# Performance work log

Measured on AMD Instinct MI355X. Metric: run time of the kernel, lower is better.

Reference implementation:

```python
import jax, jax.numpy as jnp
import numpy as np
import math

EMB = 1024
H = 8          # num_heads
HD = EMB // H // 2  # head_dim = 64
LAMBDA_INIT = 0.8
B, N = 2, 2048


def setup_inputs() -> dict:
    key = jax.random.key(0)
    ks = jax.random.split(key, 16)
    s = 1.0 / math.sqrt(EMB)
    d = {
        'q': jax.random.normal(ks[0], (B, N, EMB), jnp.float32),
        'k': jax.random.normal(ks[1], (B, N, EMB), jnp.float32),
        'v': jax.random.normal(ks[2], (B, N, EMB), jnp.float32),
        'Wq': jax.random.uniform(ks[3], (EMB, EMB), jnp.float32, -s, s),
        'bq': jax.random.uniform(ks[4], (EMB,), jnp.float32, -s, s),
        'Wk': jax.random.uniform(ks[5], (EMB, EMB), jnp.float32, -s, s),
        'bk': jax.random.uniform(ks[6], (EMB,), jnp.float32, -s, s),
        'Wv': jax.random.uniform(ks[7], (EMB, EMB), jnp.float32, -s, s),
        'bv': jax.random.uniform(ks[8], (EMB,), jnp.float32, -s, s),
        'Wo': jax.random.uniform(ks[9], (EMB, EMB), jnp.float32, -s, s),
        'bo': jax.random.uniform(ks[10], (EMB,), jnp.float32, -s, s),
        'lambda_q1': 0.1 * jax.random.normal(ks[11], (HD,), jnp.float32),
        'lambda_k1': 0.1 * jax.random.normal(ks[12], (HD,), jnp.float32),
        'lambda_q2': 0.1 * jax.random.normal(ks[13], (HD,), jnp.float32),
        'lambda_k2': 0.1 * jax.random.normal(ks[14], (HD,), jnp.float32),
    }
    return d


def reference(q, k, v, Wq, bq, Wk, bk, Wv, bv, Wo, bo,
              lambda_q1, lambda_k1, lambda_q2, lambda_k2):
    b, n, _ = q.shape
    # projections (torch Linear: x @ W.T + b)
    qp = q @ Wq.T + bq            # [b, n, EMB]
    kp = k @ Wk.T + bk
    vp = v @ Wv.T + bv
    # split into 2*H sub-heads of width HD for q/k; H heads of width 2*HD for v
    qh = qp.reshape(b, n, 2 * H, HD).transpose(0, 2, 1, 3)   # [b, 2H, n, HD]
    kh = kp.reshape(b, n, 2 * H, HD).transpose(0, 2, 1, 3)   # [b, 2H, n, HD]
    vh = vp.reshape(b, n, H, 2 * HD).transpose(0, 2, 1, 3)   # [b, H, n, 2HD]
    scale = 1.0 / math.sqrt(HD)
    attn = jnp.einsum('bhqd,bhkd->bhqk', qh, kh) * scale      # [b, 2H, n, n]
    attn = jax.nn.softmax(attn, axis=-1)
    lam1 = jnp.exp(jnp.sum(lambda_q1 * lambda_k1))
    lam2 = jnp.exp(jnp.sum(lambda_q2 * lambda_k2))
    lam = lam1 - lam2 + LAMBDA_INIT
    attn = attn.reshape(b, H, 2, n, n)
    diff = attn[:, :, 0] - lam * attn[:, :, 1]                # [b, H, n, n]
    out = jnp.einsum('bhqk,bhkd->bhqd', diff, vh)             # [b, H, n, 2HD]
    out = out.transpose(0, 2, 1, 3).reshape(b, n, H * 2 * HD)
    return out @ Wo.T + bo
```

## Files before the change

### kernel.cpp

```cpp
#include <hip/hip_runtime.h>
#include <stdint.h>


typedef __attribute__((ext_vector_type(8))) __bf16 bf16x8;
typedef __attribute__((ext_vector_type(4))) __bf16 bf16x4;
typedef __attribute__((ext_vector_type(4))) float f32x4;
typedef __attribute__((ext_vector_type(16))) float f32x16;
typedef __attribute__((ext_vector_type(8))) unsigned short u16x8;
typedef __attribute__((ext_vector_type(4))) unsigned short u16x4;
typedef __attribute__((ext_vector_type(4))) unsigned int u32x4;
typedef unsigned short u16;
typedef unsigned int u32;

#define EMB 1024
#define NSEQ 2048
#define NBATCH 2
#define NHEAD 8
#define MROWS (NBATCH*NSEQ)
#define QSCALE 0.18033688011112042f

__device__ __forceinline__ u16x4 pk4(float a, float b, float c, float d){
  bf16x4 h; h[0]=(__bf16)a; h[1]=(__bf16)b; h[2]=(__bf16)c; h[3]=(__bf16)d;
  return __builtin_bit_cast(u16x4, h);
}
__device__ __forceinline__ u16 bf1(float f){
  __bf16 h = (__bf16)f; return __builtin_bit_cast(unsigned short, h);
}
__device__ __forceinline__ u32 cvtpk(float lo, float hi){
  u32 r; asm("v_cvt_pk_bf16_f32 %0, %1, %2" : "=v"(r) : "v"(lo), "v"(hi)); return r;
}

__device__ __forceinline__ bf16x8 ld8(const u16* p){
  return __builtin_bit_cast(bf16x8, *(const u16x8*)p);
}

__device__ __forceinline__ void glds16(const u16* g, u16* l){
  __builtin_amdgcn_global_load_lds(
      (const __attribute__((address_space(1))) u32*)g,
      (__attribute__((address_space(3))) u32*)l, 16, 0, 0);
}

__global__ void cvt_k(const float* __restrict__ q, const float* __restrict__ k,
                      const float* __restrict__ v, const float* __restrict__ Wq,
                      const float* __restrict__ Wk, const float* __restrict__ Wv,
                      const float* __restrict__ Wo,
                      u16* qb, u16* kb, u16* vb, u16* Wqb, u16* Wkb, u16* Wvb, u16* Wob)
{
  const int NQ4 = (NBATCH*NSEQ*EMB)/4;
  const int NW4 = (EMB*EMB)/4;
  const int total = 3*NQ4 + 4*NW4;
  for (int i = blockIdx.x*blockDim.x + threadIdx.x; i < total; i += gridDim.x*blockDim.x){
    const float* src; u16* dst; int off;
    if (i < 3*NQ4){
      int t = i / NQ4; off = i - t*NQ4;
      src = t==0 ? q : (t==1 ? k : v);
      dst = t==0 ? qb : (t==1 ? kb : vb);
    } else {
      int j = i - 3*NQ4;
      int t = j / NW4; off = j - t*NW4;
      src = t==0 ? Wq : (t==1 ? Wk : (t==2 ? Wv : Wo));
      dst = t==0 ? Wqb : (t==1 ? Wkb : (t==2 ? Wvb : Wob));
    }
    f32x4 f = *((const f32x4*)src + off);
    *((u16x4*)dst + off) = pk4(f[0], f[1], f[2], f[3]);
  }
}

__global__ void lambda_k(const float* __restrict__ lq1, const float* __restrict__ lk1,
                         const float* __restrict__ lq2, const float* __restrict__ lk2,
                         float* lam)
{
  int l = threadIdx.x;
  float p1 = lq1[l]*lk1[l];
  float p2 = lq2[l]*lk2[l];
  #pragma unroll
  for (int m=1; m<64; m<<=1){ p1 += __shfl_xor(p1, m, 64); p2 += __shfl_xor(p2, m, 64); }
  if (l==0) lam[0] = __expf(p1) - __expf(p2) + 0.8f;
}

__device__ __forceinline__ void gemm_core(
    const u16* __restrict__ A, const u16* __restrict__ W, const float* __restrict__ bias,
    u16* __restrict__ Ybf, u16* __restrict__ Yvt, float* __restrict__ Yf, int mode,
    float oscale, u16* As, u16* Bs)
{
  const int tid = threadIdx.x, w = tid >> 6, l = tid & 63;
  const int l15 = l & 15, lg = l >> 4;
  const int m0 = blockIdx.y * 128, n0 = blockIdx.x * 128;
  const int wr = w >> 1, wc = w & 1;
  const int srow = w*16 + (l >> 2);
  const int skel = (l & 3) * 8;

  f32x4 acc[4][4] = {};

  for (int kt = 0; kt < EMB/32; ++kt){
    const int kb = kt*32 + skel;
    glds16(A + (size_t)(m0 + srow)*EMB + kb,      As + w*512);
    glds16(A + (size_t)(m0 + 64 + srow)*EMB + kb, As + 2048 + w*512);
    glds16(W + (size_t)(n0 + srow)*EMB + kb,      Bs + w*512);
    glds16(W + (size_t)(n0 + 64 + srow)*EMB + kb, Bs + 2048 + w*512);
    __syncthreads();

    bf16x8 af[4], bfr[4];
    #pragma unroll
    for (int mi=0; mi<4; ++mi) af[mi]  = ld8(As + (wr*64 + mi*16 + l15)*32 + lg*8);
    #pragma unroll
    for (int ni=0; ni<4; ++ni) bfr[ni] = ld8(Bs + (wc*64 + ni*16 + l15)*32 + lg*8);
    #pragma unroll
    for (int mi=0; mi<4; ++mi)
      #pragma unroll
      for (int ni=0; ni<4; ++ni)
        acc[mi][ni] = __builtin_amdgcn_mfma_f32_16x16x32_bf16(af[mi], bfr[ni], acc[mi][ni], 0,0,0);
    __syncthreads();
  }

  #pragma unroll
  for (int mi=0; mi<4; ++mi){
    const int mr = m0 + wr*64 + mi*16 + lg*4;
    #pragma unroll
    for (int ni=0; ni<4; ++ni){
      const int nc = n0 + wc*64 + ni*16 + l15;
      const float bvs = bias[nc]*oscale;
      if (mode == 0){
        #pragma unroll
        for (int i=0;i<4;++i) Ybf[(size_t)(mr+i)*EMB + nc] = bf1(fmaf(acc[mi][ni][i], oscale, bvs));
      } else if (mode == 1){
        const int h = nc >> 7, vd = nc & 127, bb = mr >> 11, t = mr & 2047;
        u16x4 pkv = pk4(acc[mi][ni][0]+bvs, acc[mi][ni][1]+bvs,
                        acc[mi][ni][2]+bvs, acc[mi][ni][3]+bvs);
        *(u16x4*)(Yvt + ((size_t)((bb*NHEAD + h)*128 + vd))*NSEQ + t) = pkv;
      } else {
        #pragma unroll
        for (int i=0;i<4;++i) Yf[(size_t)(mr+i)*EMB + nc] = acc[mi][ni][i] + bvs;
      }
    }
  }
}

__global__ __launch_bounds__(256) void gemm_qkv(
    const u16* qb, const u16* kb, const u16* vb,
    const u16* Wqb, const u16* Wkb, const u16* Wvb,
    const float* bq, const float* bk, const float* bv,
    u16* Qp, u16* Kp, u16* Vt)
{
  __shared__ __align__(16) u16 As[4096], Bs[4096];
  const int z = blockIdx.z;
  const u16* A = z==0 ? qb : (z==1 ? kb : vb);
  const u16* W = z==0 ? Wqb : (z==1 ? Wkb : Wvb);
  const float* bias = z==0 ? bq : (z==1 ? bk : bv);
  if (z == 0)      gemm_core(A, W, bias, Qp, nullptr, nullptr, 0, QSCALE, As, Bs);
  else if (z == 1) gemm_core(A, W, bias, Kp, nullptr, nullptr, 0, 1.0f, As, Bs);
  else             gemm_core(A, W, bias, nullptr, Vt, nullptr, 1, 1.0f, As, Bs);
}

__global__ __launch_bounds__(256) void gemm_out_k(
    const u16* Xc, const u16* Wob, const float* bo, float* out)
{
  __shared__ __align__(16) u16 As[4096], Bs[4096];
  gemm_core(Xc, Wob, bo, nullptr, nullptr, out, 2, 1.0f, As, Bs);
}

__global__ __launch_bounds__(512, 4) void attn_k(
    const u16* __restrict__ Qp, const u16* __restrict__ Kp,
    const u16* __restrict__ Vt, const float* __restrict__ lamp,
    u16* __restrict__ Xc)
{
  __shared__ __align__(16) char shm[66560];
  u16* ldsK = (u16*)shm;
  u16* ldsV = (u16*)(shm + 32768);

  const int tid = threadIdx.x, w = tid >> 6, l = tid & 63;
  const int l31 = l & 31, hl = l >> 5;
  const int qg = w & 1, s = (w >> 1) & 1, g = w >> 2;
  const int wg = w & 3;
  int bid = blockIdx.x;
  bid = (bid & 7)*64 + (bid >> 3);
  const int qt = bid & 31, bh = bid >> 5;
  const int b = bh >> 3, h = bh & 7;
  const int q0 = qt*64 + qg*32;

  const u16* Kg = Kp + ((size_t)b*NSEQ)*EMB + h*128;
  const u16* Vg = Vt + ((size_t)((b*NHEAD + h)*128))*NSEQ;

  {
  }
  const u16* qbase = Qp + (size_t)(b*NSEQ + q0 + l31)*EMB + (2*h + s)*64;
  bf16x8 qa[4];
  #pragma unroll
  for (int ks=0; ks<4; ++ks) qa[ks] = ld8(qbase + ks*16 + hl*8);

  f32x16 acc[4] = {};
  float m_run = -1e30f, l_run = 0.f;

  auto STAGE = [&](int cur, int t){
    const u16* kg = Kg + (size_t)t*32*EMB;
    u16* kd = ldsK + (g*2 + cur)*4096;
    #pragma unroll
    for (int j=0;j<2;++j){
      int row = wg*8 + j*4 + (l >> 4);
      glds16(kg + (size_t)row*EMB + (((l&15) ^ (row&15))*8), kd + (wg*8 + j*4)*128);
    }
    const u16* vg = Vg + t*32;
    u16* vd2 = ldsV + (g*2 + cur)*4096;
    #pragma unroll
    for (int j=0;j<2;++j){
      int row = wg*32 + j*16 + (l >> 2);
      glds16(vg + (size_t)row*NSEQ + (((l&3) ^ ((row>>1)&3))*8), vd2 + (wg*32 + j*16)*32);
    }
  };

  STAGE(0, g);
  __syncthreads();
  int cur = 0;

  for (int i = 0; i < 32; ++i){
    if (i+1 < 32) STAGE(cur^1, 2*(i+1) + g);

    const u16* Kb = ldsK + (g*2 + cur)*4096;
    const u16* Vb = ldsV + (g*2 + cur)*4096;

    f32x16 st = {};
    __builtin_amdgcn_s_setprio(1);
    #pragma unroll
    for (int ks=0; ks<4; ++ks){
      int c = s*8 + ks*2 + hl;
      bf16x8 kf = ld8(Kb + l31*128 + ((c ^ (l31&15))*8));
      st = __builtin_amdgcn_mfma_f32_32x32x16_bf16(kf, qa[ks], st, 0,0,0);
    }
    __builtin_amdgcn_s_setprio(0);

    float tm = fmaxf(st[0], st[1]);
    #pragma unroll
    for (int r=2; r<16; ++r) tm = fmaxf(tm, st[r]);
    tm = fmaxf(tm, __shfl_xor(tm, 32, 64));
    if (!__all(tm <= m_run + 11.5f)){
      float mn = fmaxf(m_run, tm);
      float al = exp2f(m_run - mn);
      m_run = mn; l_run *= al;
      #pragma unroll
      for (int v=0; v<4; ++v)
        #pragma unroll
        for (int r=0; r<16; ++r) acc[v][r] *= al;
    }
    float p[16];
    float ssum = 0.f;
    #pragma unroll
    for (int r=0; r<16; ++r){ p[r] = exp2f(st[r] - m_run); ssum += p[r]; }
    ssum += __shfl_xor(ssum, 32, 64);
    l_run += ssum;

    bf16x8 pa[2];
    #pragma unroll
    for (int kb=0; kb<2; ++kb){
      u32 w0 = cvtpk(p[8*kb+0], p[8*kb+1]);
      u32 w1 = cvtpk(p[8*kb+2], p[8*kb+3]);
      u32 w2 = cvtpk(p[8*kb+4], p[8*kb+5]);
      u32 w3 = cvtpk(p[8*kb+6], p[8*kb+7]);
      asm volatile("v_permlane32_swap_b32 %0, %1" : "+v"(w0), "+v"(w2));
      asm volatile("v_permlane32_swap_b32 %0, %1" : "+v"(w1), "+v"(w3));
      u32x4 t4; t4[0]=w0; t4[1]=w1; t4[2]=w2; t4[3]=w3;
      pa[kb] = __builtin_bit_cast(bf16x8, t4);
    }

    __builtin_amdgcn_s_setprio(1);
    #pragma unroll
    for (int kb=0; kb<2; ++kb)
      #pragma unroll
      for (int v=0; v<4; ++v){
        int row = v*32 + l31;
        int kc = kb*2 + hl;
        bf16x8 vf = ld8(Vb + row*32 + ((kc ^ ((row>>1)&3))*8));
        acc[v] = __builtin_amdgcn_mfma_f32_32x32x16_bf16(vf, pa[kb], acc[v], 0,0,0);
      }
    __builtin_amdgcn_s_setprio(0);

    __syncthreads();
    cur ^= 1;
  }

  float* pool = (float*)shm;
  float* ml   = (float*)(shm + 65536);
  const int slot = qg*2 + s;

  if (g == 1){
    #pragma unroll
    for (int v=0; v<4; ++v)
      #pragma unroll
      for (int rr=0; rr<4; ++rr){
        f32x4 t4; t4[0]=acc[v][rr*4+0]; t4[1]=acc[v][rr*4+1];
        t4[2]=acc[v][rr*4+2]; t4[3]=acc[v][rr*4+3];
        *(f32x4*)(pool + (((slot*4 + v)*4 + rr)*64 + l)*4) = t4;
      }
    if (hl == 0){
      ml[(slot*32 + l31)*2 + 0] = m_run;
      ml[(slot*32 + l31)*2 + 1] = l_run;
    }
  }
  __syncthreads();
  float L = 1.f;
  if (g == 0){
    float pm = ml[(slot*32 + l31)*2 + 0];
    float pl = ml[(slot*32 + l31)*2 + 1];
    float M  = fmaxf(m_run, pm);
    float a0 = exp2f(m_run - M), a1 = exp2f(pm - M);
    L = l_run*a0 + pl*a1;
    #pragma unroll
    for (int v=0; v<4; ++v)
      #pragma unroll
      for (int rr=0; rr<4; ++rr){
        f32x4 c = *(f32x4*)(pool + (((slot*4 + v)*4 + rr)*64 + l)*4);
        #pragma unroll
        for (int e=0; e<4; ++e) acc[v][rr*4+e] = acc[v][rr*4+e]*a0 + c[e]*a1;
      }
  }
  __syncthreads();
  if (g == 0 && s == 1){
    const float f = lamp[0] / L;
    #pragma unroll
    for (int v=0; v<4; ++v)
      #pragma unroll
      for (int rr=0; rr<4; ++rr){
        f32x4 t4; t4[0]=acc[v][rr*4+0]*f; t4[1]=acc[v][rr*4+1]*f;
        t4[2]=acc[v][rr*4+2]*f; t4[3]=acc[v][rr*4+3]*f;
        *(f32x4*)(pool + (((qg*4 + v)*4 + rr)*64 + l)*4) = t4;
      }
  }
  __syncthreads();
  if (g == 0 && s == 0){
    const float i0 = 1.f / L;
    #pragma unroll
    for (int v=0; v<4; ++v)
      #pragma unroll
      for (int rr=0; rr<4; ++rr){
        f32x4 c = *(f32x4*)(pool + (((qg*4 + v)*4 + rr)*64 + l)*4);
        u16x4 o = pk4(acc[v][rr*4+0]*i0 - c[0], acc[v][rr*4+1]*i0 - c[1],
                      acc[v][rr*4+2]*i0 - c[2], acc[v][rr*4+3]*i0 - c[3]);
        const int col = v*32 + rr*8 + hl*4;
        *(u16x4*)(Xc + (size_t)(b*NSEQ + q0 + l31)*EMB + h*128 + col) = o;
      }
  }
}

extern "C" void kernel_launch(void* const* d_in, const int* in_sizes, int n_in,
                              void* d_out, int out_size, void* d_ws, size_t ws_size,
                              hipStream_t stream)
{
  const float* q   = (const float*)d_in[0];
  const float* k   = (const float*)d_in[1];
  const float* v   = (const float*)d_in[2];
  const float* Wq  = (const float*)d_in[3];
  const float* bq  = (const float*)d_in[4];
  const float* Wk  = (const float*)d_in[5];
  const float* bk  = (const float*)d_in[6];
  const float* Wv  = (const float*)d_in[7];
  const float* bv  = (const float*)d_in[8];
  const float* Wo  = (const float*)d_in[9];
  const float* bo  = (const float*)d_in[10];
  const float* lq1 = (const float*)d_in[11];
  const float* lk1 = (const float*)d_in[12];
  const float* lq2 = (const float*)d_in[13];
  const float* lk2 = (const float*)d_in[14];

  const size_t NQ = (size_t)MROWS*EMB;
  const size_t NW = (size_t)EMB*EMB;
  u16* qb  = (u16*)d_ws;
  u16* kb  = qb + NQ;
  u16* vb  = kb + NQ;
  u16* Wqb = vb + NQ;
  u16* Wkb = Wqb + NW;
  u16* Wvb = Wkb + NW;
  u16* Wob = Wvb + NW;
  u16* Qp  = Wob + NW;
  u16* Kp  = Qp + NQ;
  u16* Vt  = Kp + NQ;
  u16* Xc  = Vt + NQ;
  float* lam = (float*)(Xc + NQ);

  cvt_k<<<2048, 256, 0, stream>>>(q, k, v, Wq, Wk, Wv, Wo,
                                  qb, kb, vb, Wqb, Wkb, Wvb, Wob);
  lambda_k<<<1, 64, 0, stream>>>(lq1, lk1, lq2, lk2, lam);
  gemm_qkv<<<dim3(EMB/128, MROWS/128, 3), 256, 0, stream>>>(
      qb, kb, vb, Wqb, Wkb, Wvb, bq, bk, bv, Qp, Kp, Vt);
  attn_k<<<dim3(NBATCH*NHEAD*(NSEQ/64)), 512, 0, stream>>>(Qp, Kp, Vt, lam, Xc);
  gemm_out_k<<<dim3(EMB/128, MROWS/128), 256, 0, stream>>>(Xc, Wob, bo, (float*)d_out);
}
```

Baseline: 163.5 us.

## Fuse fp32-to-bf16 activation conversion into QKV GEMM A-tile loads

Removes the separate conversion pass over q/k/v. The QKV GEMM now reads fp32 activations directly, converts them to bf16 in registers and writes them to LDS, so only the weights are converted up front. This avoids writing and re-reading three bf16 activation copies. In exchange, the GEMM A-loads become synchronous register loads instead of async global-to-LDS copies, and each tile loads twice the bytes. The change also templatizes the GEMM mode, rewrites the attention max/sum reductions as trees, and drops volatile from the permlane asm.

After: 182.7 us. +11.8%, slower.

```diff
diff --git a/kernel.cpp b/kernel.cpp
--- a/kernel.cpp
+++ b/kernel.cpp
@@ -26,6 +26,12 @@
 __device__ __forceinline__ u16 bf1(float f){
   __bf16 h = (__bf16)f; return __builtin_bit_cast(unsigned short, h);
 }
+__device__ __forceinline__ u16x8 pk8(f32x4 a, f32x4 b){
+  u16x8 r;
+  r[0]=bf1(a[0]); r[1]=bf1(a[1]); r[2]=bf1(a[2]); r[3]=bf1(a[3]);
+  r[4]=bf1(b[0]); r[5]=bf1(b[1]); r[6]=bf1(b[2]); r[7]=bf1(b[3]);
+  return r;
+}
 __device__ __forceinline__ u32 cvtpk(float lo, float hi){
   u32 r; asm("v_cvt_pk_bf16_f32 %0, %1, %2" : "=v"(r) : "v"(lo), "v"(hi)); return r;
 }
@@ -40,27 +46,16 @@
       (__attribute__((address_space(3))) u32*)l, 16, 0, 0);
 }
 
-__global__ void cvt_k(const float* __restrict__ q, const float* __restrict__ k,
-                      const float* __restrict__ v, const float* __restrict__ Wq,
-                      const float* __restrict__ Wk, const float* __restrict__ Wv,
-                      const float* __restrict__ Wo,
-                      u16* qb, u16* kb, u16* vb, u16* Wqb, u16* Wkb, u16* Wvb, u16* Wob)
-{
-  const int NQ4 = (NBATCH*NSEQ*EMB)/4;
+__global__ void cvt_w(const float* __restrict__ Wq, const float* __restrict__ Wk,
+                      const float* __restrict__ Wv, const float* __restrict__ Wo,
+                      u16* Wqb, u16* Wkb, u16* Wvb, u16* Wob)
+{
   const int NW4 = (EMB*EMB)/4;
-  const int total = 3*NQ4 + 4*NW4;
+  const int total = 4*NW4;
   for (int i = blockIdx.x*blockDim.x + threadIdx.x; i < total; i += gridDim.x*blockDim.x){
-    const float* src; u16* dst; int off;
-    if (i < 3*NQ4){
-      int t = i / NQ4; off = i - t*NQ4;
-      src = t==0 ? q : (t==1 ? k : v);
-      dst = t==0 ? qb : (t==1 ? kb : vb);
-    } else {
-      int j = i - 3*NQ4;
-      int t = j / NW4; off = j - t*NW4;
-      src = t==0 ? Wq : (t==1 ? Wk : (t==2 ? Wv : Wo));
-      dst = t==0 ? Wqb : (t==1 ? Wkb : (t==2 ? Wvb : Wob));
-    }
+    int t = i / NW4, off = i - t*NW4;
+    const float* src = t==0 ? Wq : (t==1 ? Wk : (t==2 ? Wv : Wo));
+    u16* dst        = t==0 ? Wqb : (t==1 ? Wkb : (t==2 ? Wvb : Wob));
     f32x4 f = *((const f32x4*)src + off);
     *((u16x4*)dst + off) = pk4(f[0], f[1], f[2], f[3]);
   }
@@ -78,9 +73,10 @@
   if (l==0) lam[0] = __expf(p1) - __expf(p2) + 0.8f;
 }
 
+template<int MODE, bool AF32>
 __device__ __forceinline__ void gemm_core(
-    const u16* __restrict__ A, const u16* __restrict__ W, const float* __restrict__ bias,
-    u16* __restrict__ Ybf, u16* __restrict__ Yvt, float* __restrict__ Yf, int mode,
+    const void* __restrict__ Aptr, const u16* __restrict__ W, const float* __restrict__ bias,
+    u16* __restrict__ Ybf, u16* __restrict__ Yvt, float* __restrict__ Yf,
     float oscale, u16* As, u16* Bs)
 {
   const int tid = threadIdx.x, w = tid >> 6, l = tid & 63;
@@ -90,14 +86,28 @@
   const int srow = w*16 + (l >> 2);
   const int skel = (l & 3) * 8;
 
+  const float* Af = (const float*)Aptr;
+  const u16*   Ab = (const u16*)Aptr;
+
   f32x4 acc[4][4] = {};
 
   for (int kt = 0; kt < EMB/32; ++kt){
     const int kb = kt*32 + skel;
-    glds16(A + (size_t)(m0 + srow)*EMB + kb,      As + w*512);
-    glds16(A + (size_t)(m0 + 64 + srow)*EMB + kb, As + 2048 + w*512);
-    glds16(W + (size_t)(n0 + srow)*EMB + kb,      Bs + w*512);
-    glds16(W + (size_t)(n0 + 64 + srow)*EMB + kb, Bs + 2048 + w*512);
+    if constexpr (AF32){
+      const float* p0 = Af + (size_t)(m0 + srow)*EMB + kb;
+      const float* p1 = Af + (size_t)(m0 + 64 + srow)*EMB + kb;
+      f32x4 a0 = *(const f32x4*)p0, a1 = *(const f32x4*)(p0+4);
+      f32x4 a2 = *(const f32x4*)p1, a3 = *(const f32x4*)(p1+4);
+      glds16(W + (size_t)(n0 + srow)*EMB + kb,      Bs + w*512);
+      glds16(W + (size_t)(n0 + 64 + srow)*EMB + kb, Bs + 2048 + w*512);
+      *(u16x8*)(As + srow*32 + skel)        = pk8(a0, a1);
+      *(u16x8*)(As + 2048 + srow*32 + skel) = pk8(a2, a3);
+    } else {
+      glds16(Ab + (size_t)(m0 + srow)*EMB + kb,      As + w*512);
+      glds16(Ab + (size_t)(m0 + 64 + srow)*EMB + kb, As + 2048 + w*512);
+      glds16(W + (size_t)(n0 + srow)*EMB + kb,      Bs + w*512);
+      glds16(W + (size_t)(n0 + 64 + srow)*EMB + kb, Bs + 2048 + w*512);
+    }
     __syncthreads();
 
     bf16x8 af[4], bfr[4];
@@ -120,10 +130,10 @@
     for (int ni=0; ni<4; ++ni){
       const int nc = n0 + wc*64 + ni*16 + l15;
       const float bvs = bias[nc]*oscale;
-      if (mode == 0){
+      if constexpr (MODE == 0){
         #pragma unroll
         for (int i=0;i<4;++i) Ybf[(size_t)(mr+i)*EMB + nc] = bf1(fmaf(acc[mi][ni][i], oscale, bvs));
-      } else if (mode == 1){
+      } else if constexpr (MODE == 1){
         const int h = nc >> 7, vd = nc & 127, bb = mr >> 11, t = mr & 2047;
         u16x4 pkv = pk4(acc[mi][ni][0]+bvs, acc[mi][ni][1]+bvs,
                         acc[mi][ni][2]+bvs, acc[mi][ni][3]+bvs);
@@ -137,26 +147,23 @@
 }
 
 __global__ __launch_bounds__(256) void gemm_qkv(
-    const u16* qb, const u16* kb, const u16* vb,
+    const float* qf, const float* kf, const float* vf,
     const u16* Wqb, const u16* Wkb, const u16* Wvb,
     const float* bq, const float* bk, const float* bv,
     u16* Qp, u16* Kp, u16* Vt)
 {
   __shared__ __align__(16) u16 As[4096], Bs[4096];
   const int z = blockIdx.z;
-  const u16* A = z==0 ? qb : (z==1 ? kb : vb);
-  const u16* W = z==0 ? Wqb : (z==1 ? Wkb : Wvb);
-  const float* bias = z==0 ? bq : (z==1 ? bk : bv);
-  if (z == 0)      gemm_core(A, W, bias, Qp, nullptr, nullptr, 0, QSCALE, As, Bs);
-  else if (z == 1) gemm_core(A, W, bias, Kp, nullptr, nullptr, 0, 1.0f, As, Bs);
-  else             gemm_core(A, W, bias, nullptr, Vt, nullptr, 1, 1.0f, As, Bs);
+  if (z == 0)      gemm_core<0,true>(qf, Wqb, bq, Qp, nullptr, nullptr, QSCALE, As, Bs);
+  else if (z == 1) gemm_core<0,true>(kf, Wkb, bk, Kp, nullptr, nullptr, 1.0f, As, Bs);
+  else             gemm_core<1,true>(vf, Wvb, bv, nullptr, Vt, nullptr, 1.0f, As, Bs);
 }
 
 __global__ __launch_bounds__(256) void gemm_out_k(
     const u16* Xc, const u16* Wob, const float* bo, float* out)
 {
   __shared__ __align__(16) u16 As[4096], Bs[4096];
-  gemm_core(Xc, Wob, bo, nullptr, nullptr, out, 2, 1.0f, As, Bs);
+  gemm_core<2,false>(Xc, Wob, bo, nullptr, nullptr, out, 1.0f, As, Bs);
 }
 
 __global__ __launch_bounds__(512, 4) void attn_k(
@@ -181,8 +188,6 @@
   const u16* Kg = Kp + ((size_t)b*NSEQ)*EMB + h*128;
   const u16* Vg = Vt + ((size_t)((b*NHEAD + h)*128))*NSEQ;
 
-  {
-  }
   const u16* qbase = Qp + (size_t)(b*NSEQ + q0 + l31)*EMB + (2*h + s)*64;
   bf16x8 qa[4];
   #pragma unroll
@@ -228,9 +233,12 @@
     }
     __builtin_amdgcn_s_setprio(0);
 
-    float tm = fmaxf(st[0], st[1]);
-    #pragma unroll
-    for (int r=2; r<16; ++r) tm = fmaxf(tm, st[r]);
+    float t0 = fmaxf(fmaxf(st[0], st[1]), st[2]);
+    float t1 = fmaxf(fmaxf(st[3], st[4]), st[5]);
+    float t2 = fmaxf(fmaxf(st[6], st[7]), st[8]);
+    float t3 = fmaxf(fmaxf(st[9], st[10]), st[11]);
+    float t4 = fmaxf(fmaxf(st[12], st[13]), st[14]);
+    float tm = fmaxf(fmaxf(fmaxf(t0, t1), t2), fmaxf(fmaxf(t3, t4), st[15]));
     tm = fmaxf(tm, __shfl_xor(tm, 32, 64));
     if (!__all(tm <= m_run + 11.5f)){
       float mn = fmaxf(m_run, tm);
@@ -242,9 +250,13 @@
         for (int r=0; r<16; ++r) acc[v][r] *= al;
     }
     float p[16];
-    float ssum = 0.f;
-    #pragma unroll
-    for (int r=0; r<16; ++r){ p[r] = exp2f(st[r] - m_run); ssum += p[r]; }
+    #pragma unroll
+    for (int r=0; r<16; ++r) p[r] = exp2f(st[r] - m_run);
+    float s0 = (p[0]+p[1]) + (p[2]+p[3]);
+    float s1 = (p[4]+p[5]) + (p[6]+p[7]);
+    float s2 = (p[8]+p[9]) + (p[10]+p[11]);
+    float s3 = (p[12]+p[13]) + (p[14]+p[15]);
+    float ssum = (s0+s1) + (s2+s3);
     ssum += __shfl_xor(ssum, 32, 64);
     l_run += ssum;
 
@@ -255,8 +267,8 @@
       u32 w1 = cvtpk(p[8*kb+2], p[8*kb+3]);
       u32 w2 = cvtpk(p[8*kb+4], p[8*kb+5]);
       u32 w3 = cvtpk(p[8*kb+6], p[8*kb+7]);
-      asm volatile("v_permlane32_swap_b32 %0, %1" : "+v"(w0), "+v"(w2));
-      asm volatile("v_permlane32_swap_b32 %0, %1" : "+v"(w1), "+v"(w3));
+      asm("v_permlane32_swap_b32 %0, %1" : "+v"(w0), "+v"(w2));
+      asm("v_permlane32_swap_b32 %0, %1" : "+v"(w1), "+v"(w3));
       u32x4 t4; t4[0]=w0; t4[1]=w1; t4[2]=w2; t4[3]=w3;
       pa[kb] = __builtin_bit_cast(bf16x8, t4);
     }
@@ -362,10 +374,7 @@
 
   const size_t NQ = (size_t)MROWS*EMB;
   const size_t NW = (size_t)EMB*EMB;
-  u16* qb  = (u16*)d_ws;
-  u16* kb  = qb + NQ;
-  u16* vb  = kb + NQ;
-  u16* Wqb = vb + NQ;
+  u16* Wqb = (u16*)d_ws;
   u16* Wkb = Wqb + NW;
   u16* Wvb = Wkb + NW;
   u16* Wob = Wvb + NW;
@@ -375,11 +384,10 @@
   u16* Xc  = Vt + NQ;
   float* lam = (float*)(Xc + NQ);
 
-  cvt_k<<<2048, 256, 0, stream>>>(q, k, v, Wq, Wk, Wv, Wo,
-                                  qb, kb, vb, Wqb, Wkb, Wvb, Wob);
+  cvt_w<<<1024, 256, 0, stream>>>(Wq, Wk, Wv, Wo, Wqb, Wkb, Wvb, Wob);
   lambda_k<<<1, 64, 0, stream>>>(lq1, lk1, lq2, lk2, lam);
   gemm_qkv<<<dim3(EMB/128, MROWS/128, 3), 256, 0, stream>>>(
-      qb, kb, vb, Wqb, Wkb, Wvb, bq, bk, bv, Qp, Kp, Vt);
+      q, k, v, Wqb, Wkb, Wvb, bq, bk, bv, Qp, Kp, Vt);
   attn_k<<<dim3(NBATCH*NHEAD*(NSEQ/64)), 512, 0, stream>>>(Qp, Kp, Vt, lam, Xc);
   gemm_out_k<<<dim3(EMB/128, MROWS/128), 256, 0, stream>>>(Xc, Wob, bo, (float*)d_out);
 }
```
